# Kernel optimization log

Measured on AMD Instinct MI355X. Metric: run time of the kernel, lower is better.

Reference implementation:

```python
import jax, jax.numpy as jnp
import numpy as np

B, L, HID = 8, 1025, 1024
H, KV, DH = 16, 4, 64
EPS = 1e-6
ROPE_BASE = 10000.0


def _rms_norm(x, w):
    var = jnp.mean(jnp.square(x), axis=-1, keepdims=True)
    return x * jax.lax.rsqrt(var + EPS) * w


def _rotate_half(x):
    x1, x2 = jnp.split(x, 2, axis=-1)
    return jnp.concatenate([-x2, x1], axis=-1)


def _rope_cache(seq_len, dim):
    inv_freq = 1.0 / (ROPE_BASE ** (jnp.arange(0, dim, 2, dtype=jnp.float32) / dim))
    pos = jnp.arange(seq_len, dtype=jnp.float32)
    freqs = pos[:, None] * inv_freq[None, :]            # [L_img, dim/2]
    emb = jnp.concatenate([freqs, freqs], axis=-1)       # [L_img, dim]
    return jnp.cos(emb), jnp.sin(emb)


def setup_inputs() -> dict:
    key = jax.random.key(0)
    ks = jax.random.split(key, 5)
    s_in = 1.0
    s_q = float(np.sqrt(2.0 / (HID + H * DH)))
    s_kv = float(np.sqrt(2.0 / (HID + KV * DH)))
    s_o = float(np.sqrt(2.0 / (H * DH + HID)) / np.sqrt(2.0))
    return {
        "inputs": jax.random.normal(ks[0], (B, L, HID), jnp.float32) * s_in,
        "Wq": jax.random.normal(ks[1], (H * DH, HID), jnp.float32) * s_q,
        "Wk": jax.random.normal(ks[2], (KV * DH, HID), jnp.float32) * s_kv,
        "Wv": jax.random.normal(ks[3], (KV * DH, HID), jnp.float32) * s_kv,
        "Wo": jax.random.normal(ks[4], (HID, H * DH), jnp.float32) * s_o,
        "q_norm_w": jnp.ones((DH,), jnp.float32),
        "k_norm_w": jnp.ones((DH,), jnp.float32),
    }


def reference(inputs, Wq, Wk, Wv, Wo, q_norm_w, k_norm_w):
    b, l, _ = inputs.shape
    # projections (torch Linear: x @ W.T), reshape to heads, QK RMSNorm
    q = (inputs @ Wq.T).reshape(b, l, H, DH)
    k = (inputs @ Wk.T).reshape(b, l, KV, DH)
    v = (inputs @ Wv.T).reshape(b, l, KV, DH)
    q = _rms_norm(q, q_norm_w).transpose(0, 2, 1, 3)    # [B,H,L,DH]
    k = _rms_norm(k, k_norm_w).transpose(0, 2, 1, 3)    # [B,KV,L,DH]
    v = v.transpose(0, 2, 1, 3)                          # [B,KV,L,DH]

    # RoPE only on image tokens (skip first action token)
    l_img = l - 1
    cos, sin = _rope_cache(l_img, DH)                    # [L_img, DH]
    cos = cos[None, None].astype(q.dtype)
    sin = sin[None, None].astype(q.dtype)
    q_img = q[:, :, 1:]
    k_img = k[:, :, 1:]
    q = jnp.concatenate([q[:, :, :1], q_img * cos + _rotate_half(q_img) * sin], axis=2)
    k = jnp.concatenate([k[:, :, :1], k_img * cos + _rotate_half(k_img) * sin], axis=2)

    # GQA: repeat kv heads
    rep = H // KV
    k = jnp.repeat(k, rep, axis=1)                       # [B,H,L,DH]
    v = jnp.repeat(v, rep, axis=1)

    # manual attention: NOTE no 1/sqrt(DH) scaling (faithful to source)
    scores = jnp.einsum("bhqd,bhkd->bhqk", q, k)
    attn = jax.nn.softmax(scores.astype(jnp.float32), axis=-1).astype(q.dtype)
    out = jnp.einsum("bhqk,bhkd->bhqd", attn, v)         # [B,H,L,DH]
    out = out.transpose(0, 2, 1, 3).reshape(b, l, H * DH)
    return out @ Wo.T
```

## Files before the change

kernel.cpp:

```cpp
#include <hip/hip_runtime.h>
#include <hip/hip_bf16.h>

using bf16 = __hip_bfloat16;
typedef __bf16 bf16x8 __attribute__((ext_vector_type(8)));
typedef float f32x4 __attribute__((ext_vector_type(4)));
typedef short short8 __attribute__((ext_vector_type(8)));
typedef unsigned short ushort4v __attribute__((ext_vector_type(4)));

#define MFMA16(a, b, c) __builtin_amdgcn_mfma_f32_16x16x32_bf16((a), (b), (c), 0, 0, 0)

constexpr int B_ = 8, L_ = 1025, H_ = 16, KV_ = 4;
constexpr int LKP_ = 1088;
constexpr int M_ = B_ * L_;

constexpr int NX = 8396800, NWQ = 1048576, NWK = 262144, NWV = 262144,
              NWO = 1048576, NNW = 64;

__device__ __forceinline__ void gl_lds16(const bf16* g, bf16* l) {
  __builtin_amdgcn_global_load_lds(
      (const __attribute__((address_space(1))) void*)g,
      (__attribute__((address_space(3))) void*)l, 16, 0, 0);
}

template <int NWG>
__device__ __forceinline__ int xcd_swz(int orig) {
  constexpr int q = NWG >> 3, r = NWG & 7;
  const int x = orig & 7, idx = orig >> 3;
  return (x < r ? x * (q + 1) : r * (q + 1) + (x - r) * q) + idx;
}

__global__ __launch_bounds__(64) void detect_dtype(const unsigned short* qw_raw,
                                                   int* flag) {
  if (threadIdx.x == 0) flag[0] = (qw_raw[0] == 0x3F80) ? 0 : 1;
}

__global__ __launch_bounds__(256) void convert_all(
    const void* s0, const void* s1, const void* s2, const void* s3,
    const void* s4, const void* s5, const void* s6,
    bf16* d0, bf16* d1, bf16* d2, bf16* d3, bf16* d4, bf16* d5, bf16* d6,
    const int* flag) {
  const int f = *flag;
  const int tid = blockIdx.x * blockDim.x + threadIdx.x;
  const int stride = gridDim.x * blockDim.x;
  auto conv = [&](const void* s, bf16* d, int n) {
    const int n8 = n >> 3;
    if (f) {
      const f32x4* sf = (const f32x4*)s;
      short8* dd = (short8*)d;
      for (int i = tid; i < n8; i += stride) {
        const f32x4 v0 = sf[2 * i], v1 = sf[2 * i + 1];
        short8 o;
#pragma unroll
        for (int j = 0; j < 4; ++j) {
          o[j]     = __builtin_bit_cast(short, __float2bfloat16(v0[j]));
          o[j + 4] = __builtin_bit_cast(short, __float2bfloat16(v1[j]));
        }
        dd[i] = o;
      }
    } else {
      const short8* su = (const short8*)s;
      short8* dd = (short8*)d;
      for (int i = tid; i < n8; i += stride) dd[i] = su[i];
    }
  };
  conv(s0, d0, NX);
  conv(s1, d1, NWQ);
  conv(s2, d2, NWK);
  conv(s3, d3, NWV);
  conv(s4, d4, NWO);
  conv(s5, d5, NNW);
  conv(s6, d6, NNW);
}

__global__ __launch_bounds__(256) void zero_pads(bf16* Kb, bf16* VT) {
  const int idx = blockIdx.x * 256 + threadIdx.x;
  const bf16 z = __float2bfloat16(0.f);
  {
    const int g = idx / 4032, rem = idx % 4032;
    const int r = rem >> 6, d = rem & 63;
    Kb[((size_t)g * LKP_ + 1025 + r) * 64 + d] = z;
  }
  {
    const int row = idx / 63, c = idx % 63;
    VT[(size_t)row * LKP_ + 1025 + c] = z;
  }
}

template <int EPI, int NT, int NWG>
__global__ __launch_bounds__(512) void gemm_bt(
    const bf16* __restrict__ X, const bf16* __restrict__ W0,
    const bf16* __restrict__ W1, const bf16* __restrict__ W2,
    void* __restrict__ O0, bf16* __restrict__ O1, bf16* __restrict__ O2,
    const bf16* __restrict__ qw, const bf16* __restrict__ kw,
    const int* flag) {
  const int wg = xcd_swz<NWG>(blockIdx.x);
  const int m0 = (wg / NT) * 128;
  const int n0 = (wg % NT) * 128;

  int outf32 = 0;
  if constexpr (EPI == 0) outf32 = *flag;

  const bf16* W;
  int nw0;
  if constexpr (EPI == 0) {
    W = W0; nw0 = n0;
  } else {
    if (n0 < 1024)      { W = W0; nw0 = n0; }
    else if (n0 < 1280) { W = W1; nw0 = n0 - 1024; }
    else                { W = W2; nw0 = n0 - 1280; }
  }

  __shared__ bf16 As[3][128 * 32];
  __shared__ bf16 Bs[3][128 * 32];

  const int tid = threadIdx.x;
  const int lane = tid & 63, wid = tid >> 6;
  const int wr = wid >> 1, wc = wid & 1;
  const int lo = lane & 15, g = lane >> 4;

  const f32x4 zero4 = {0.f, 0.f, 0.f, 0.f};
  f32x4 acc[2][4];
#pragma unroll
  for (int i = 0; i < 2; ++i)
#pragma unroll
    for (int j = 0; j < 4; ++j) acc[i][j] = zero4;

  const int rr = tid >> 2;
  const int csw = ((tid & 3) ^ ((rr >> 1) & 3)) * 8;
  int xr = m0 + rr; if (xr > M_ - 1) xr = M_ - 1;
  const bf16* xp = X + (size_t)xr * 1024 + csw;
  const bf16* wp = W + (size_t)(nw0 + rr) * 1024 + csw;

  auto stage = [&](int buf) {
    gl_lds16(xp, &As[buf][(size_t)tid * 8]);
    gl_lds16(wp, &Bs[buf][(size_t)tid * 8]);
    xp += 32; wp += 32;
  };

  stage(0);
  stage(1);

  const int swl = (g ^ ((lo >> 1) & 3)) * 8;

  for (int kt = 0; kt < 32; ++kt) {
    if (kt < 31) asm volatile("s_waitcnt vmcnt(2)" ::: "memory");
    else         asm volatile("s_waitcnt vmcnt(0)" ::: "memory");
    __builtin_amdgcn_s_barrier();
    if (kt < 30) stage((kt + 2) % 3);

    const int cur = kt % 3;
    bf16x8 a[2], bb[4];
#pragma unroll
    for (int i = 0; i < 2; ++i)
      a[i] = *reinterpret_cast<const bf16x8*>(&As[cur][(wr * 32 + i * 16 + lo) * 32 + swl]);
#pragma unroll
    for (int j = 0; j < 4; ++j)
      bb[j] = *reinterpret_cast<const bf16x8*>(&Bs[cur][(wc * 64 + j * 16 + lo) * 32 + swl]);
#pragma unroll
    for (int i = 0; i < 2; ++i)
#pragma unroll
      for (int j = 0; j < 4; ++j)
        acc[i][j] = MFMA16(a[i], bb[j], acc[i][j]);
  }

  const bool qkreg = (EPI == 1) && (n0 < 1280);
  float wv[4];
  float invf0 = 0.f, invf1 = 0.f;
  if (qkreg) {
    const bf16* w = (n0 < 1024) ? qw : kw;
#pragma unroll
    for (int j = 0; j < 4; ++j) wv[j] = __bfloat162float(w[j * 16 + lo]);
    constexpr float c = -0.41524101186092029f;
    invf0 = exp2f((float)lo * c);
    invf1 = invf0 * exp2f(16.f * c);
  }

#pragma unroll
  for (int i = 0; i < 2; ++i) {
#pragma unroll
    for (int ii = 0; ii < 4; ++ii) {
      const int m = m0 + wr * 32 + i * 16 + g * 4 + ii;
      if (m >= M_) continue;
      const int b = m / L_;
      const int l = m % L_;
      float fv[4];
#pragma unroll
      for (int j = 0; j < 4; ++j) fv[j] = acc[i][j][ii];

      if (qkreg) {
#pragma unroll
        for (int j = 0; j < 4; ++j)
          fv[j] = __bfloat162float(__float2bfloat16(fv[j]));
        float ss = fv[0] * fv[0] + fv[1] * fv[1] + fv[2] * fv[2] + fv[3] * fv[3];
        ss += __shfl_xor(ss, 1);
        ss += __shfl_xor(ss, 2);
        ss += __shfl_xor(ss, 4);
        ss += __shfl_xor(ss, 8);
        const float r = rsqrtf(ss * (1.f / 64.f) + 1e-6f);
#pragma unroll
        for (int j = 0; j < 4; ++j) fv[j] *= r * wv[j];
        if (l > 0) {
          const float pos = (float)(l - 1);
          float sn0, cs0, sn1, cs1;
          __sincosf(pos * invf0, &sn0, &cs0);
          __sincosf(pos * invf1, &sn1, &cs1);
          const float a0 = fv[0], a2 = fv[2];
          fv[0] = a0 * cs0 - a2 * sn0;
          fv[2] = a2 * cs0 + a0 * sn0;
          const float a1 = fv[1], a3 = fv[3];
          fv[1] = a1 * cs1 - a3 * sn1;
          fv[3] = a3 * cs1 + a1 * sn1;
        }
      }

#pragma unroll
      for (int j = 0; j < 4; ++j) {
        const int n = n0 + wc * 64 + j * 16 + lo;
        const float f = fv[j];
        if constexpr (EPI == 0) {
          if (outf32) ((float*)O0)[(size_t)m * 1024 + n] = f;
          else        ((bf16*)O0)[(size_t)m * 1024 + n] = __float2bfloat16(f);
        } else {
          const bf16 v = __float2bfloat16(f);
          if (n < 1024) {
            ((bf16*)O0)[((size_t)(b * H_ + (n >> 6)) * L_ + l) * 64 + (n & 63)] = v;
          } else if (n < 1280) {
            const int c2 = n - 1024;
            O1[((size_t)(b * KV_ + (c2 >> 6)) * LKP_ + l) * 64 + (c2 & 63)] = v;
          } else {
            const int c2 = n - 1280;
            O2[((size_t)(b * KV_ + (c2 >> 6)) * 64 + (c2 & 63)) * LKP_ + l] = v;
          }
        }
      }
    }
  }
}

__global__ __launch_bounds__(512) void attn(
    const bf16* __restrict__ Q, const bf16* __restrict__ Kt,
    const bf16* __restrict__ VT, bf16* __restrict__ AO) {
  const int tid = threadIdx.x, lane = tid & 63, w = tid >> 6;
  const int lo = lane & 15, g = lane >> 4;
  const int qt = blockIdx.x, h = blockIdx.y, b = blockIdx.z;
  const int kv = h >> 2;

  __shared__ unsigned short Ks[64 * 64];
  __shared__ unsigned short Vs[64 * 64];
  __shared__ unsigned short Ps[8 * 16 * 64];

  const bf16* qbase = Q + (size_t)(b * H_ + h) * L_ * 64;
  int qrow = qt * 128 + w * 16 + lo;
  if (qrow > L_ - 1) qrow = L_ - 1;
  const bf16x8 qf0 = *reinterpret_cast<const bf16x8*>(qbase + (size_t)qrow * 64 + g * 8);
  const bf16x8 qf1 = *reinterpret_cast<const bf16x8*>(qbase + (size_t)qrow * 64 + 32 + g * 8);

  const f32x4 zero4 = {0.f, 0.f, 0.f, 0.f};
  f32x4 o[4];
  float mi = -3e38f, li = 0.f;
#pragma unroll
  for (int i = 0; i < 4; ++i) o[i] = zero4;

  const int sr = tid >> 3;
  const int scol = (tid & 7) * 8;
  const int swcol = ((tid & 7) ^ (sr & 7)) * 8;
  const bf16* kptr = Kt + ((size_t)(b * KV_ + kv) * LKP_ + sr) * 64 + scol;
  const bf16* vptr = VT + ((size_t)(b * KV_ + kv) * 64 + sr) * LKP_ + scol;

  const int sw0 = (g ^ (lo & 7)) * 8;
  const int sw1 = ((4 | g) ^ (lo & 7)) * 8;

  short8 ka = *reinterpret_cast<const short8*>(kptr);
  short8 va = *reinterpret_cast<const short8*>(vptr);

  for (int kt = 0; kt < 17; ++kt) {
    __syncthreads();
    *reinterpret_cast<short8*>(&Ks[sr * 64 + swcol]) = ka;
    *reinterpret_cast<short8*>(&Vs[sr * 64 + swcol]) = va;
    __syncthreads();

    if (kt < 16) {
      kptr += 64 * 64;
      vptr += 64;
      ka = *reinterpret_cast<const short8*>(kptr);
      va = *reinterpret_cast<const short8*>(vptr);
    }

    f32x4 s[4];
    __builtin_amdgcn_s_setprio(1);
#pragma unroll
    for (int kb = 0; kb < 4; ++kb) {
      f32x4 t = zero4;
      const bf16x8 ka0 = *reinterpret_cast<const bf16x8*>(&Ks[(kb * 16 + lo) * 64 + sw0]);
      const bf16x8 ka1 = *reinterpret_cast<const bf16x8*>(&Ks[(kb * 16 + lo) * 64 + sw1]);
      t = MFMA16(ka0, qf0, t);
      t = MFMA16(ka1, qf1, t);
      s[kb] = t;
    }
    __builtin_amdgcn_s_setprio(0);
    if (kt == 16) {
#pragma unroll
      for (int kb = 0; kb < 4; ++kb)
#pragma unroll
        for (int i = 0; i < 4; ++i)
          if (kt * 64 + kb * 16 + g * 4 + i >= L_) s[kb][i] = -1e30f;
    }

    float t0 = fmaxf(fmaxf(s[0][0], s[0][1]), fmaxf(s[0][2], s[0][3]));
    float t1 = fmaxf(fmaxf(s[1][0], s[1][1]), fmaxf(s[1][2], s[1][3]));
    float t2 = fmaxf(fmaxf(s[2][0], s[2][1]), fmaxf(s[2][2], s[2][3]));
    float t3 = fmaxf(fmaxf(s[3][0], s[3][1]), fmaxf(s[3][2], s[3][3]));
    float tm = fmaxf(fmaxf(t0, t1), fmaxf(t2, t3));
    tm = fmaxf(tm, __shfl_xor(tm, 16));
    tm = fmaxf(tm, __shfl_xor(tm, 32));
    if (!__all(tm <= mi)) {
      const float mn = fmaxf(mi, tm);
      const float sc = __expf(mi - mn);
      mi = mn;
      li *= sc;
#pragma unroll
      for (int db = 0; db < 4; ++db)
#pragma unroll
        for (int i = 0; i < 4; ++i) o[db][i] *= sc;
    }
#pragma unroll
    for (int kb = 0; kb < 4; ++kb)
#pragma unroll
      for (int i = 0; i < 4; ++i) s[kb][i] = __expf(s[kb][i] - mi);
    float p0 = (s[0][0] + s[0][1]) + (s[0][2] + s[0][3]);
    float p1 = (s[1][0] + s[1][1]) + (s[1][2] + s[1][3]);
    float p2 = (s[2][0] + s[2][1]) + (s[2][2] + s[2][3]);
    float p3 = (s[3][0] + s[3][1]) + (s[3][2] + s[3][3]);
    float ps = (p0 + p1) + (p2 + p3);
    ps += __shfl_xor(ps, 16);
    ps += __shfl_xor(ps, 32);
    li += ps;

#pragma unroll
    for (int kb = 0; kb < 4; ++kb) {
      ushort4v pk;
#pragma unroll
      for (int i = 0; i < 4; ++i)
        pk[i] = __builtin_bit_cast(unsigned short, __float2bfloat16(s[kb][i]));
      const int pblk = (2 * kb + (g >> 1)) ^ (lo & 7);
      *reinterpret_cast<ushort4v*>(&Ps[w * 1024 + lo * 64 + pblk * 8 + (g & 1) * 4]) = pk;
    }

    const bf16x8 pb0 = *reinterpret_cast<const bf16x8*>(&Ps[w * 1024 + lo * 64 + sw0]);
    const bf16x8 pb1 = *reinterpret_cast<const bf16x8*>(&Ps[w * 1024 + lo * 64 + sw1]);
    __builtin_amdgcn_s_setprio(1);
#pragma unroll
    for (int db = 0; db < 4; ++db) {
      const bf16x8 va0 = *reinterpret_cast<const bf16x8*>(&Vs[(db * 16 + lo) * 64 + sw0]);
      const bf16x8 va1 = *reinterpret_cast<const bf16x8*>(&Vs[(db * 16 + lo) * 64 + sw1]);
      o[db] = MFMA16(va0, pb0, o[db]);
      o[db] = MFMA16(va1, pb1, o[db]);
    }
    __builtin_amdgcn_s_setprio(0);
  }

  const int qr = qt * 128 + w * 16 + lo;
  if (qr < L_) {
    const float inv = 1.f / li;
    unsigned* base = (unsigned*)(AO + ((size_t)b * L_ + qr) * 1024 + h * 64);
#pragma unroll
    for (int db = 0; db < 4; ++db) {
#pragma unroll
      for (int i2 = 0; i2 < 4; i2 += 2) {
        const unsigned u0 = __builtin_bit_cast(unsigned short,
                                __float2bfloat16(o[db][i2] * inv));
        const unsigned u1 = __builtin_bit_cast(unsigned short,
                                __float2bfloat16(o[db][i2 + 1] * inv));
        base[(db * 16 + 4 * g + i2) >> 1] = u0 | (u1 << 16);
      }
    }
  }
}

extern "C" void kernel_launch(void* const* d_in, const int* in_sizes, int n_in,
                              void* d_out, int out_size, void* d_ws, size_t ws_size,
                              hipStream_t stream) {
  (void)in_sizes; (void)n_in; (void)out_size; (void)ws_size;

  char* wsb = (char*)d_ws;
  int* flagp = (int*)wsb;
  bf16* cX  = (bf16*)(wsb + 16);
  bf16* cWq = cX + NX;
  bf16* cWk = cWq + NWQ;
  bf16* cWv = cWk + NWK;
  bf16* cWo = cWv + NWV;
  bf16* cqw = cWo + NWO;
  bf16* ckw = cqw + NNW;
  bf16* Qb  = ckw + NNW;
  bf16* Kb  = Qb  + (size_t)B_ * H_ * L_ * 64;
  bf16* VTb = Kb  + (size_t)B_ * KV_ * LKP_ * 64;
  bf16* AOb = VTb + (size_t)B_ * KV_ * 64 * LKP_;

  detect_dtype<<<1, 64, 0, stream>>>((const unsigned short*)d_in[5], flagp);
  convert_all<<<2048, 256, 0, stream>>>(
      d_in[0], d_in[1], d_in[2], d_in[3], d_in[4], d_in[5], d_in[6],
      cX, cWq, cWk, cWv, cWo, cqw, ckw, flagp);
  zero_pads<<<504, 256, 0, stream>>>(Kb, VTb);

  gemm_bt<1, 12, 780><<<780, 512, 0, stream>>>(cX, cWq, cWk, cWv, Qb, Kb, VTb,
                                               cqw, ckw, nullptr);
  attn<<<dim3(9, 16, 8), 512, 0, stream>>>(Qb, Kb, VTb, AOb);
  gemm_bt<0, 8, 520><<<520, 512, 0, stream>>>(AOb, cWo, nullptr, nullptr, d_out,
                                              nullptr, nullptr, nullptr, nullptr,
                                              flagp);
}
```

Before: 216.1 us.

## Use larger GEMM tiles with split-K phase pipelining and skip bf16 copy conversion

Replaces the 128x128 triple-buffered GEMM with a 256-wide N tile (BM 256 for QKV, 128 for output projection), double buffered with two K-half phases per 64-wide step. It adds a new LDS swizzle, dummy loads so the vmcnt waits stay constant, and raised MFMA priority. The conversion kernel now returns early for bf16 inputs, and the GEMMs read the raw inputs directly instead of copying them. The norm weights are read straight from the inputs. The larger tiles reduce the block count (198 and 260 blocks), which risks underfilling the GPU's compute units. The f32 conversion path is now scalar rather than vectorized.

```diff
diff --git a/kernel.cpp b/kernel.cpp
--- a/kernel.cpp
+++ b/kernel.cpp
@@ -14,7 +14,7 @@
 constexpr int M_ = B_ * L_;
 
 constexpr int NX = 8396800, NWQ = 1048576, NWK = 262144, NWV = 262144,
-              NWO = 1048576, NNW = 64;
+              NWO = 1048576;
 
 __device__ __forceinline__ void gl_lds16(const bf16* g, bf16* l) {
   __builtin_amdgcn_global_load_lds(
@@ -34,42 +34,23 @@
   if (threadIdx.x == 0) flag[0] = (qw_raw[0] == 0x3F80) ? 0 : 1;
 }
 
-__global__ __launch_bounds__(256) void convert_all(
+__global__ __launch_bounds__(256) void convert_f32(
     const void* s0, const void* s1, const void* s2, const void* s3,
-    const void* s4, const void* s5, const void* s6,
-    bf16* d0, bf16* d1, bf16* d2, bf16* d3, bf16* d4, bf16* d5, bf16* d6,
-    const int* flag) {
-  const int f = *flag;
+    const void* s4,
+    bf16* d0, bf16* d1, bf16* d2, bf16* d3, bf16* d4,
+    const int* __restrict__ flag) {
+  if (*flag == 0) return;
   const int tid = blockIdx.x * blockDim.x + threadIdx.x;
   const int stride = gridDim.x * blockDim.x;
   auto conv = [&](const void* s, bf16* d, int n) {
-    const int n8 = n >> 3;
-    if (f) {
-      const f32x4* sf = (const f32x4*)s;
-      short8* dd = (short8*)d;
-      for (int i = tid; i < n8; i += stride) {
-        const f32x4 v0 = sf[2 * i], v1 = sf[2 * i + 1];
-        short8 o;
-#pragma unroll
-        for (int j = 0; j < 4; ++j) {
-          o[j]     = __builtin_bit_cast(short, __float2bfloat16(v0[j]));
-          o[j + 4] = __builtin_bit_cast(short, __float2bfloat16(v1[j]));
-        }
-        dd[i] = o;
-      }
-    } else {
-      const short8* su = (const short8*)s;
-      short8* dd = (short8*)d;
-      for (int i = tid; i < n8; i += stride) dd[i] = su[i];
-    }
+    const float* sf = (const float*)s;
+    for (int i = tid; i < n; i += stride) d[i] = __float2bfloat16(sf[i]);
   };
   conv(s0, d0, NX);
   conv(s1, d1, NWQ);
   conv(s2, d2, NWK);
   conv(s3, d3, NWV);
   conv(s4, d4, NWO);
-  conv(s5, d5, NNW);
-  conv(s6, d6, NNW);
 }
 
 __global__ __launch_bounds__(256) void zero_pads(bf16* Kb, bf16* VT) {
@@ -86,100 +67,146 @@
   }
 }
 
-template <int EPI, int NT, int NWG>
-__global__ __launch_bounds__(512) void gemm_bt(
-    const bf16* __restrict__ X, const bf16* __restrict__ W0,
-    const bf16* __restrict__ W1, const bf16* __restrict__ W2,
+template <int EPI, int BM, int NT, int NWG>
+__global__ __launch_bounds__(512, 1) void gemm8p(
+    const bf16* __restrict__ Araw, const bf16* __restrict__ Aconv,
+    const bf16* __restrict__ W0r, const bf16* __restrict__ W0c,
+    const bf16* __restrict__ W1r, const bf16* __restrict__ W1c,
+    const bf16* __restrict__ W2r, const bf16* __restrict__ W2c,
     void* __restrict__ O0, bf16* __restrict__ O1, bf16* __restrict__ O2,
-    const bf16* __restrict__ qw, const bf16* __restrict__ kw,
-    const int* flag) {
+    const void* __restrict__ qwv, const void* __restrict__ kwv,
+    const int* __restrict__ flag) {
+  constexpr int MSPAN = BM / 2;
+  constexpr int M_REP = BM / 32;
+  constexpr int LA = BM / 128;
+  constexpr int AOFF_ = 0;
+  constexpr int BOFF_ = BM * 128;
+  constexpr int DOFF_ = BOFF_ + 32768;
+  constexpr int LDSZ_ = DOFF_ + 4096;
+
+  const int f32in = *flag;
   const int wg = xcd_swz<NWG>(blockIdx.x);
-  const int m0 = (wg / NT) * 128;
-  const int n0 = (wg % NT) * 128;
-
-  int outf32 = 0;
-  if constexpr (EPI == 0) outf32 = *flag;
-
-  const bf16* W;
+  const int m0 = (wg / NT) * BM;
+  const int n0 = (wg % NT) * 256;
+
+  const bf16* A = (EPI == 0) ? Araw : (f32in ? Aconv : Araw);
+  const bf16 *Wr, *Wc;
   int nw0;
   if constexpr (EPI == 0) {
-    W = W0; nw0 = n0;
+    Wr = W0r; Wc = W0c; nw0 = n0;
   } else {
-    if (n0 < 1024)      { W = W0; nw0 = n0; }
-    else if (n0 < 1280) { W = W1; nw0 = n0 - 1024; }
-    else                { W = W2; nw0 = n0 - 1280; }
-  }
-
-  __shared__ bf16 As[3][128 * 32];
-  __shared__ bf16 Bs[3][128 * 32];
-
-  const int tid = threadIdx.x;
-  const int lane = tid & 63, wid = tid >> 6;
-  const int wr = wid >> 1, wc = wid & 1;
+    if (n0 < 1024)      { Wr = W0r; Wc = W0c; nw0 = n0; }
+    else if (n0 < 1280) { Wr = W1r; Wc = W1c; nw0 = n0 - 1024; }
+    else                { Wr = W2r; Wc = W2c; nw0 = n0 - 1280; }
+  }
+  const bf16* W = f32in ? Wc : Wr;
+
+  __shared__ bf16 lds[LDSZ_];
+
+  const int tid = threadIdx.x, lane = tid & 63, wid = tid >> 6;
+  const int wr = wid >> 2, wc = wid & 3;
   const int lo = lane & 15, g = lane >> 4;
 
   const f32x4 zero4 = {0.f, 0.f, 0.f, 0.f};
-  f32x4 acc[2][4];
-#pragma unroll
-  for (int i = 0; i < 2; ++i)
+  f32x4 acc[M_REP][4];
+#pragma unroll
+  for (int i = 0; i < M_REP; ++i)
 #pragma unroll
     for (int j = 0; j < 4; ++j) acc[i][j] = zero4;
 
-  const int rr = tid >> 2;
-  const int csw = ((tid & 3) ^ ((rr >> 1) & 3)) * 8;
-  int xr = m0 + rr; if (xr > M_ - 1) xr = M_ - 1;
-  const bf16* xp = X + (size_t)xr * 1024 + csw;
-  const bf16* wp = W + (size_t)(nw0 + rr) * 1024 + csw;
-
-  auto stage = [&](int buf) {
-    gl_lds16(xp, &As[buf][(size_t)tid * 8]);
-    gl_lds16(wp, &Bs[buf][(size_t)tid * 8]);
-    xp += 32; wp += 32;
+  auto stage = [&](int kt, int ks) {
+    const bool dum = (kt > 15);
+    const int kc = dum ? 15 : kt;
+    const int buf = kt & 1;
+    const int kbase = kc * 64 + ks * 32;
+#pragma unroll
+    for (int c = 0; c < LA; ++c) {
+      const int idx8 = c * 512 + tid;
+      const int band = idx8 / (BM * 2);
+      const int rem = idx8 - band * (BM * 2);
+      const int r = rem >> 1, hh = rem & 1;
+      const int hl = hh ^ ((r >> 2) & 1);
+      int xr = m0 + r; if (xr > M_ - 1) xr = M_ - 1;
+      const bf16* src = A + (size_t)xr * 1024 + kbase + band * 16 + hl * 8;
+      bf16* dst = dum ? &lds[DOFF_ + (size_t)tid * 8]
+                      : &lds[AOFF_ + ((buf * 4 + 2 * ks) * BM) * 16 + (size_t)idx8 * 8];
+      gl_lds16(src, dst);
+    }
+#pragma unroll
+    for (int c = 0; c < 2; ++c) {
+      const int idx8 = c * 512 + tid;
+      const int band = idx8 >> 9;
+      const int rem = idx8 & 511;
+      const int r = rem >> 1, hh = rem & 1;
+      const int hl = hh ^ ((r >> 2) & 1);
+      const bf16* src = W + (size_t)(nw0 + r) * 1024 + kbase + band * 16 + hl * 8;
+      bf16* dst = dum ? &lds[DOFF_ + (size_t)tid * 8]
+                      : &lds[BOFF_ + ((buf * 4 + 2 * ks) * 256) * 16 + (size_t)idx8 * 8];
+      gl_lds16(src, dst);
+    }
   };
 
-  stage(0);
-  stage(1);
-
-  const int swl = (g ^ ((lo >> 1) & 3)) * 8;
-
-  for (int kt = 0; kt < 32; ++kt) {
-    if (kt < 31) asm volatile("s_waitcnt vmcnt(2)" ::: "memory");
-    else         asm volatile("s_waitcnt vmcnt(0)" ::: "memory");
+  auto phase = [&](int kt, int ks) {
+    if constexpr (BM == 256) asm volatile("s_waitcnt vmcnt(8)" ::: "memory");
+    else                     asm volatile("s_waitcnt vmcnt(6)" ::: "memory");
     __builtin_amdgcn_s_barrier();
-    if (kt < 30) stage((kt + 2) % 3);
-
-    const int cur = kt % 3;
-    bf16x8 a[2], bb[4];
-#pragma unroll
-    for (int i = 0; i < 2; ++i)
-      a[i] = *reinterpret_cast<const bf16x8*>(&As[cur][(wr * 32 + i * 16 + lo) * 32 + swl]);
-#pragma unroll
-    for (int j = 0; j < 4; ++j)
-      bb[j] = *reinterpret_cast<const bf16x8*>(&Bs[cur][(wc * 64 + j * 16 + lo) * 32 + swl]);
-#pragma unroll
-    for (int i = 0; i < 2; ++i)
+    __builtin_amdgcn_sched_barrier(0);
+    const int buf = kt & 1;
+    const int bnd = buf * 4 + 2 * ks + (g >> 1);
+    bf16x8 af[M_REP], bb[4];
+#pragma unroll
+    for (int i = 0; i < M_REP; ++i) {
+      const int row = wr * MSPAN + i * 16 + lo;
+      const int hp = (g & 1) ^ ((row >> 2) & 1);
+      af[i] = *reinterpret_cast<const bf16x8*>(&lds[AOFF_ + (bnd * BM + row) * 16 + hp * 8]);
+    }
+#pragma unroll
+    for (int j = 0; j < 4; ++j) {
+      const int row = wc * 64 + j * 16 + lo;
+      const int hp = (g & 1) ^ ((row >> 2) & 1);
+      bb[j] = *reinterpret_cast<const bf16x8*>(&lds[BOFF_ + (bnd * 256 + row) * 16 + hp * 8]);
+    }
+    if (ks == 0) stage(kt + 1, 1);
+    else         stage(kt + 2, 0);
+    asm volatile("s_waitcnt lgkmcnt(0)" ::: "memory");
+    __builtin_amdgcn_sched_barrier(0);
+    __builtin_amdgcn_s_setprio(1);
+#pragma unroll
+    for (int i = 0; i < M_REP; ++i)
 #pragma unroll
       for (int j = 0; j < 4; ++j)
-        acc[i][j] = MFMA16(a[i], bb[j], acc[i][j]);
-  }
-
-  const bool qkreg = (EPI == 1) && (n0 < 1280);
+        acc[i][j] = MFMA16(af[i], bb[j], acc[i][j]);
+    __builtin_amdgcn_s_setprio(0);
+  };
+
+  stage(0, 0); stage(0, 1); stage(1, 0);
+  for (int kt = 0; kt < 16; ++kt) {
+    phase(kt, 0);
+    phase(kt, 1);
+  }
+  asm volatile("s_waitcnt vmcnt(0)" ::: "memory");
+
+  const bool qkreg = (EPI == 1) && (n0 + wc * 64 < 1280);
   float wv[4];
   float invf0 = 0.f, invf1 = 0.f;
   if (qkreg) {
-    const bf16* w = (n0 < 1024) ? qw : kw;
-#pragma unroll
-    for (int j = 0; j < 4; ++j) wv[j] = __bfloat162float(w[j * 16 + lo]);
-    constexpr float c = -0.41524101186092029f;
-    invf0 = exp2f((float)lo * c);
-    invf1 = invf0 * exp2f(16.f * c);
-  }
-
-#pragma unroll
-  for (int i = 0; i < 2; ++i) {
+    const void* w = (n0 + wc * 64 < 1024) ? qwv : kwv;
+#pragma unroll
+    for (int j = 0; j < 4; ++j) {
+      float wf = f32in ? ((const float*)w)[j * 16 + lo]
+                       : __bfloat162float(((const bf16*)w)[j * 16 + lo]);
+      wv[j] = __bfloat162float(__float2bfloat16(wf));
+    }
+    constexpr float cc = -0.41524101186092029f;
+    invf0 = exp2f((float)lo * cc);
+    invf1 = invf0 * exp2f(16.f * cc);
+  }
+
+#pragma unroll
+  for (int i = 0; i < M_REP; ++i) {
 #pragma unroll
     for (int ii = 0; ii < 4; ++ii) {
-      const int m = m0 + wr * 32 + i * 16 + g * 4 + ii;
+      const int m = m0 + wr * MSPAN + i * 16 + g * 4 + ii;
       if (m >= M_) continue;
       const int b = m / L_;
       const int l = m % L_;
@@ -218,8 +245,8 @@
         const int n = n0 + wc * 64 + j * 16 + lo;
         const float f = fv[j];
         if constexpr (EPI == 0) {
-          if (outf32) ((float*)O0)[(size_t)m * 1024 + n] = f;
-          else        ((bf16*)O0)[(size_t)m * 1024 + n] = __float2bfloat16(f);
+          if (f32in) ((float*)O0)[(size_t)m * 1024 + n] = f;
+          else       ((bf16*)O0)[(size_t)m * 1024 + n] = __float2bfloat16(f);
         } else {
           const bf16 v = __float2bfloat16(f);
           if (n < 1024) {
@@ -389,23 +416,26 @@
   bf16* cWk = cWq + NWQ;
   bf16* cWv = cWk + NWK;
   bf16* cWo = cWv + NWV;
-  bf16* cqw = cWo + NWO;
-  bf16* ckw = cqw + NNW;
-  bf16* Qb  = ckw + NNW;
+  bf16* Qb  = cWo + NWO;
   bf16* Kb  = Qb  + (size_t)B_ * H_ * L_ * 64;
   bf16* VTb = Kb  + (size_t)B_ * KV_ * LKP_ * 64;
   bf16* AOb = VTb + (size_t)B_ * KV_ * 64 * LKP_;
 
+  const bf16* X  = (const bf16*)d_in[0];
+  const bf16* Wq = (const bf16*)d_in[1];
+  const bf16* Wk = (const bf16*)d_in[2];
+  const bf16* Wv = (const bf16*)d_in[3];
+  const bf16* Wo = (const bf16*)d_in[4];
+
   detect_dtype<<<1, 64, 0, stream>>>((const unsigned short*)d_in[5], flagp);
-  convert_all<<<2048, 256, 0, stream>>>(
-      d_in[0], d_in[1], d_in[2], d_in[3], d_in[4], d_in[5], d_in[6],
-      cX, cWq, cWk, cWv, cWo, cqw, ckw, flagp);
+  convert_f32<<<2048, 256, 0, stream>>>(d_in[0], d_in[1], d_in[2], d_in[3],
+                                        d_in[4], cX, cWq, cWk, cWv, cWo, flagp);
   zero_pads<<<504, 256, 0, stream>>>(Kb, VTb);
 
-  gemm_bt<1, 12, 780><<<780, 512, 0, stream>>>(cX, cWq, cWk, cWv, Qb, Kb, VTb,
-                                               cqw, ckw, nullptr);
+  gemm8p<1, 256, 6, 198><<<198, 512, 0, stream>>>(
+      X, cX, Wq, cWq, Wk, cWk, Wv, cWv, Qb, Kb, VTb, d_in[5], d_in[6], flagp);
   attn<<<dim3(9, 16, 8), 512, 0, stream>>>(Qb, Kb, VTb, AOb);
-  gemm_bt<0, 8, 520><<<520, 512, 0, stream>>>(AOb, cWo, nullptr, nullptr, d_out,
-                                              nullptr, nullptr, nullptr, nullptr,
-                                              flagp);
-}
+  gemm8p<0, 128, 4, 260><<<260, 512, 0, stream>>>(
+      AOb, AOb, Wo, cWo, nullptr, nullptr, nullptr, nullptr, d_out,
+      nullptr, nullptr, nullptr, nullptr, flagp);
+}
```

New measurement: 228.5 us. +5.7%, slower.
